# Performance work log

Hardware: AMD Instinct MI355X
Metric: run time of the kernel (lower is better)

The kernel has to match this reference:

```python
import jax, jax.numpy as jnp
import numpy as np

M, T, D, H = 2, 2048, 1024, 16
HD = D // H
SCALE = 1.0 / np.sqrt(D).astype(np.float32)  # original divides by sqrt(emb_dim)


def setup_inputs() -> dict:
    key = jax.random.key(0)
    ks = jax.random.split(key, 8)
    def lin(k):
        kw, kb = jax.random.split(k)
        W = jax.random.normal(kw, (D, D), dtype=jnp.float32) * (1.0 / np.sqrt(D))
        b = jax.random.normal(kb, (D,), dtype=jnp.float32) * 0.01
        return W, b
    Wq, bq = lin(ks[0]); Wk, bk = lin(ks[1]); Wv, bv = lin(ks[2]); Wo, bo = lin(ks[3])
    Q = jax.random.normal(ks[4], (M, T, D), dtype=jnp.float32)
    K = jax.random.normal(ks[5], (M, T, D), dtype=jnp.float32)
    V = jax.random.normal(ks[6], (M, T, D), dtype=jnp.float32)
    mask = jnp.ones((M, 1, 1, T), dtype=jnp.int32)
    return {"Q": Q, "K": K, "V": V, "mask": mask,
            "Wq": Wq, "bq": bq, "Wk": Wk, "bk": bk,
            "Wv": Wv, "bv": bv, "Wo": Wo, "bo": bo}


def reference(Q, K, V, mask, Wq, bq, Wk, bk, Wv, bv, Wo, bo):
    m = Q.shape[0]
    # torch nn.Linear: y = x @ W.T + b
    q = (Q @ Wq.T + bq).reshape(m, -1, H, HD)  # (m, Tq, h, hd)
    k = (K @ Wk.T + bk).reshape(m, -1, H, HD)
    v = (V @ Wv.T + bv).reshape(m, -1, H, HD)
    energy = jnp.einsum('mqhd,mkhd->mhqk', q, k) * SCALE
    if mask is not None:
        energy = jnp.where(mask == 0, jnp.float32(-1e20), energy)
    attn = jax.nn.softmax(energy, axis=3)  # dropout is identity at inference
    out = jnp.einsum('mhqk,mkhd->mqhd', attn, v)  # (m, Tq, h, hd)
    concat = out.reshape(m, -1, H * HD)
    return concat @ Wo.T + bo
```

## Files before the change

kernel.cpp:

```cpp
#include <hip/hip_runtime.h>
#include <cstdint>
#include <cstddef>

#define T_SEQ 2048
#define D_EMB 1024
#define H_HEADS 16
#define MROWS 4096
#define SC2 (0.03125f * 1.44269504f)
#define MASKNEG (-1e30f)

typedef __attribute__((ext_vector_type(8))) short bf16x8;
typedef __attribute__((ext_vector_type(4))) float f32x4;
typedef __attribute__((ext_vector_type(16))) float f32x16;
typedef __attribute__((ext_vector_type(4))) unsigned short us4;

__device__ __forceinline__ unsigned short f2bf(float f) {
  union { float f; uint32_t u; } v; v.f = f;
  uint32_t u = v.u;
  return (unsigned short)((u + 0x7FFFu + ((u >> 16) & 1u)) >> 16);
}

__device__ __forceinline__ uint32_t cvtpk(float lo, float hi) {
  uint32_t r;
  asm("v_cvt_pk_bf16_f32 %0, %1, %2" : "=v"(r) : "v"(lo), "v"(hi));
  return r;
}

__device__ __forceinline__ float fexp2(float x) {
  float r;
  asm("v_exp_f32 %0, %1" : "=v"(r) : "v"(x));
  return r;
}

__device__ __forceinline__ void gl16(const void* g, void* l) {
  __builtin_amdgcn_global_load_lds(
      (const __attribute__((address_space(1))) unsigned int*)g,
      (__attribute__((address_space(3))) unsigned int*)l, 16, 0, 0);
}

__global__ __launch_bounds__(256) void cvt_all(
    const float* __restrict__ Q, const float* __restrict__ K, const float* __restrict__ V,
    const float* __restrict__ Wq, const float* __restrict__ Wk,
    const float* __restrict__ Wv, const float* __restrict__ Wo,
    unsigned short* __restrict__ Qb, unsigned short* __restrict__ Kb,
    unsigned short* __restrict__ Vb,
    unsigned short* __restrict__ Wqb, unsigned short* __restrict__ Wkb,
    unsigned short* __restrict__ Wvb, unsigned short* __restrict__ Wob) {
  int i = blockIdx.x * 256 + threadIdx.x;
  const float* src;
  unsigned short* dst;
  int j;
  if (i < 3145728) {
    int s = i >> 20;
    j = i & 1048575;
    src = (s == 0) ? Q : (s == 1) ? K : V;
    dst = (s == 0) ? Qb : (s == 1) ? Kb : Vb;
  } else {
    int k = i - 3145728;
    int s = k >> 18;
    j = k & 262143;
    src = (s == 0) ? Wq : (s == 1) ? Wk : (s == 2) ? Wv : Wo;
    dst = (s == 0) ? Wqb : (s == 1) ? Wkb : (s == 2) ? Wvb : Wob;
  }
  float4 f = ((const float4*)src)[j];
  us4 o;
  o[0] = f2bf(f.x); o[1] = f2bf(f.y); o[2] = f2bf(f.z); o[3] = f2bf(f.w);
  ((us4*)dst)[j] = o;
}

__global__ __launch_bounds__(256) void qkv_gemm(
    const unsigned short* __restrict__ Qb, const unsigned short* __restrict__ Kb,
    const unsigned short* __restrict__ Vb,
    const unsigned short* __restrict__ Wqb, const unsigned short* __restrict__ Wkb,
    const unsigned short* __restrict__ Wvb,
    const float* __restrict__ bq, const float* __restrict__ bk, const float* __restrict__ bv,
    unsigned short* __restrict__ qo, unsigned short* __restrict__ ko,
    unsigned short* __restrict__ vto) {
  const int swz = (blockIdx.x & 7) * 96 + (blockIdx.x >> 3);
  const int bx = swz & 7, by = (swz >> 3) & 31, z = swz >> 8;
  const unsigned short* A = (z == 0) ? Qb : (z == 1) ? Kb : Vb;
  const unsigned short* W = (z == 0) ? Wqb : (z == 1) ? Wkb : Wvb;
  const float* bias = (z == 0) ? bq : (z == 1) ? bk : bv;

  __shared__ __align__(16) unsigned short Asm[2][128 * 32];
  __shared__ __align__(16) unsigned short Bsm[2][128 * 32];

  const int tid = threadIdx.x;
  const int lane = tid & 63, w = tid >> 6;
  const int fq = lane >> 4, fr = lane & 15;
  const int brow = by * 128, bcol = bx * 128;
  const int wr = (w >> 1) * 64, wc = (w & 1) * 64;

  f32x4 acc[4][4] = {};

#define QKV_STAGE(buf, k0)                                                     \
  {                                                                            \
    _Pragma("unroll") for (int it = 0; it < 2; ++it) {                         \
      int idx = it * 256 + tid;                                                \
      int row = idx >> 2, ce = (idx & 3) * 8;                                  \
      gl16(&A[(size_t)(brow + row) * D_EMB + (k0) + ce],                       \
           (char*)Asm[buf] + idx * 16);                                        \
      gl16(&W[(size_t)(bcol + row) * D_EMB + (k0) + ce],                       \
           (char*)Bsm[buf] + idx * 16);                                        \
    }                                                                          \
  }

#define QKV_COMPUTE(buf)                                                       \
  {                                                                            \
    bf16x8 af[4], bfr[4];                                                      \
    _Pragma("unroll") for (int i = 0; i < 4; ++i)                              \
        af[i] = *(const bf16x8*)((const char*)Asm[buf] +                       \
                                 (wr + i * 16 + fr) * 64 + fq * 16);           \
    _Pragma("unroll") for (int j = 0; j < 4; ++j)                              \
        bfr[j] = *(const bf16x8*)((const char*)Bsm[buf] +                      \
                                  (wc + j * 16 + fr) * 64 + fq * 16);          \
    _Pragma("unroll") for (int i = 0; i < 4; ++i)                              \
        _Pragma("unroll") for (int j = 0; j < 4; ++j)                          \
            acc[i][j] = __builtin_amdgcn_mfma_f32_16x16x32_bf16(               \
                af[i], bfr[j], acc[i][j], 0, 0, 0);                            \
  }

  QKV_STAGE(0, 0);
  __syncthreads();
#pragma unroll 1
  for (int t = 0; t < 32; t += 2) {
    QKV_STAGE(1, (t + 1) * 32);
    QKV_COMPUTE(0);
    __syncthreads();
    if (t + 2 < 32) QKV_STAGE(0, (t + 2) * 32);
    QKV_COMPUTE(1);
    __syncthreads();
  }

#pragma unroll
  for (int i = 0; i < 4; ++i) {
#pragma unroll
    for (int j = 0; j < 4; ++j) {
      int r0 = brow + wr + i * 16 + fq * 4;
      int cc = bcol + wc + j * 16 + fr;
      float bb = bias[cc];
      if (z < 2) {
        unsigned short* O = (z == 0) ? qo : ko;
        float sc = (z == 0) ? SC2 : 1.0f;
#pragma unroll
        for (int q = 0; q < 4; ++q)
          O[(size_t)(r0 + q) * D_EMB + cc] = f2bf((acc[i][j][q] + bb) * sc);
      } else {
        int hh = cc >> 6, dd = cc & 63;
        int mm = r0 >> 11, tt = r0 & 2047;
        us4 pk;
#pragma unroll
        for (int q = 0; q < 4; ++q) pk[q] = f2bf(acc[i][j][q] + bb);
        *(us4*)&vto[((size_t)((mm * H_HEADS + hh) * 64 + dd)) * T_SEQ + tt] = pk;
      }
    }
  }
}

__global__ __launch_bounds__(256) void out_gemm(const unsigned short* __restrict__ Ab,
                                                const unsigned short* __restrict__ Wb,
                                                const float* __restrict__ bias,
                                                float* __restrict__ Out) {
  const int swz = (blockIdx.x & 7) * 64 + (blockIdx.x >> 3);
  const int bx = swz & 15, by = swz >> 4;

  __shared__ __align__(16) unsigned short Asm[2][128 * 32];
  __shared__ __align__(16) unsigned short Bsm[2][64 * 32];
  const int tid = threadIdx.x;
  const int lane = tid & 63, w = tid >> 6;
  const int fq = lane >> 4, fr = lane & 15;
  const int brow = by * 128, bcol = bx * 64;
  const int wr = w * 32;

  f32x4 acc[2][4] = {};

#define OUT_STAGE(buf, k0)                                                     \
  {                                                                            \
    _Pragma("unroll") for (int it = 0; it < 2; ++it) {                         \
      int idx = it * 256 + tid;                                                \
      int row = idx >> 2, ce = (idx & 3) * 8;                                  \
      gl16(&Ab[(size_t)(brow + row) * D_EMB + (k0) + ce],                      \
           (char*)Asm[buf] + idx * 16);                                        \
    }                                                                          \
    {                                                                          \
      int row = tid >> 2, ce = (tid & 3) * 8;                                  \
      gl16(&Wb[(size_t)(bcol + row) * D_EMB + (k0) + ce],                      \
           (char*)Bsm[buf] + tid * 16);                                        \
    }                                                                          \
  }

#define OUT_COMPUTE(buf)                                                       \
  {                                                                            \
    bf16x8 af[2], bfr[4];                                                      \
    _Pragma("unroll") for (int i = 0; i < 2; ++i)                              \
        af[i] = *(const bf16x8*)((const char*)Asm[buf] +                       \
                                 (wr + i * 16 + fr) * 64 + fq * 16);           \
    _Pragma("unroll") for (int j = 0; j < 4; ++j)                              \
        bfr[j] = *(const bf16x8*)((const char*)Bsm[buf] +                      \
                                  (j * 16 + fr) * 64 + fq * 16);               \
    _Pragma("unroll") for (int i = 0; i < 2; ++i)                              \
        _Pragma("unroll") for (int j = 0; j < 4; ++j)                          \
            acc[i][j] = __builtin_amdgcn_mfma_f32_16x16x32_bf16(               \
                af[i], bfr[j], acc[i][j], 0, 0, 0);                            \
  }

  OUT_STAGE(0, 0);
  __syncthreads();
#pragma unroll 1
  for (int t = 0; t < 32; t += 2) {
    OUT_STAGE(1, (t + 1) * 32);
    OUT_COMPUTE(0);
    __syncthreads();
    if (t + 2 < 32) OUT_STAGE(0, (t + 2) * 32);
    OUT_COMPUTE(1);
    __syncthreads();
  }

#pragma unroll
  for (int i = 0; i < 2; ++i)
#pragma unroll
    for (int j = 0; j < 4; ++j) {
      int r0 = brow + wr + i * 16 + fq * 4;
      int cc = bcol + j * 16 + fr;
      float bb = bias[cc];
#pragma unroll
      for (int q = 0; q < 4; ++q)
        Out[(size_t)(r0 + q) * D_EMB + cc] = acc[i][j][q] + bb;
    }
}

__global__ __launch_bounds__(256) void attn_fwd(const unsigned short* __restrict__ qb,
                                                const unsigned short* __restrict__ kb,
                                                const unsigned short* __restrict__ vtb,
                                                const int* __restrict__ maskg,
                                                unsigned short* __restrict__ outb) {
  const int swzb = (blockIdx.x & 7) * 64 + (blockIdx.x >> 3);
  const int qt = swzb & 15, h = (swzb >> 4) & 15, mI = swzb >> 8;
  const int tid = threadIdx.x;
  const int lane = tid & 63, w = tid >> 6;
  const int lq = lane & 31, h2 = lane >> 5;
  const int xk = (lq & 7) << 4;
  const int vx = (lq & 7) << 4;

  __shared__ __align__(16) unsigned short Ksm[128 * 64];
  __shared__ __align__(16) unsigned short Vsm[64 * 128];
  __shared__ __align__(16) char Pw[4][2304];
  __shared__ __align__(16) float Msm[128];
  __shared__ int moks[16];

  char* KsmB = (char*)Ksm;
  char* VsmB = (char*)Vsm;
  char* PwB = Pw[w];

  if (tid < 16) moks[tid] = 1;
  __syncthreads();
  {
    int bad = 0;
    const int4* mg = (const int4*)&maskg[mI * T_SEQ + tid * 8];
    int4 a = mg[0], b = mg[1];
    bad |= (a.x == 0) | (a.y == 0) | (a.z == 0) | (a.w == 0);
    bad |= (b.x == 0) | (b.y == 0) | (b.z == 0) | (b.w == 0);
    if (bad) moks[tid >> 4] = 0;
  }
  __syncthreads();
  int okbits = 0;
#pragma unroll
  for (int i = 0; i < 16; ++i) okbits |= (moks[i] != 0) << i;

  const int qrow = qt * 128 + w * 32 + lq;
  bf16x8 qf[4];
#pragma unroll
  for (int db = 0; db < 4; ++db)
    qf[db] = *(const bf16x8*)&qb[((size_t)(mI * T_SEQ) + qrow) * D_EMB + h * 64 + db * 16 + h2 * 8];

  f32x16 oacc[2] = {};
  f32x16 liv = {};

  const unsigned short* kpan = kb + (size_t)(mI * T_SEQ) * D_EMB + h * 64;
  const unsigned short* vpan = vtb + (size_t)(mI * H_HEADS + h) * 64 * T_SEQ;

#pragma unroll 1
  for (int k0 = 0; k0 < T_SEQ; k0 += 128) {
    const int ok = (okbits >> (k0 >> 7)) & 1;
#pragma unroll
    for (int it = 0; it < 4; ++it) {
      int idx = it * 256 + tid;
      int row = idx >> 3;
      int sb = ((idx & 7) * 16) ^ ((row & 7) << 4);
      gl16(kpan + (size_t)(k0 + row) * D_EMB + (sb >> 1), KsmB + idx * 16);
    }
#pragma unroll
    for (int it = 0; it < 4; ++it) {
      int idx = it * 256 + tid;
      int row = idx >> 4;
      int sb = ((idx & 15) * 16) ^ ((row & 7) << 4);
      gl16(vpan + (size_t)row * T_SEQ + k0 + (sb >> 1), VsmB + idx * 16);
    }
    if (!ok && tid < 128) Msm[tid] = (maskg[mI * T_SEQ + k0 + tid] == 0) ? MASKNEG : 0.f;
    __syncthreads();

#pragma unroll 1
    for (int kbk = 0; kbk < 4; ++kbk) {
      f32x16 sv = {};
      const char* kr = KsmB + (kbk * 32 + lq) * 128;
#pragma unroll
      for (int db = 0; db < 4; ++db) {
        bf16x8 kf = *(const bf16x8*)(kr + ((db * 32 + h2 * 16) ^ xk));
        sv = __builtin_amdgcn_mfma_f32_32x32x16_bf16(kf, qf[db], sv, 0, 0, 0);
      }
      if (!ok) {
#pragma unroll
        for (int rg = 0; rg < 4; ++rg) {
          f32x4 mk = *(const f32x4*)&Msm[kbk * 32 + rg * 8 + h2 * 4];
          sv[rg * 4 + 0] += mk[0]; sv[rg * 4 + 1] += mk[1];
          sv[rg * 4 + 2] += mk[2]; sv[rg * 4 + 3] += mk[3];
        }
      }
#pragma unroll
      for (int r = 0; r < 16; ++r) sv[r] = fexp2(sv[r]);
      liv += sv;
#pragma unroll
      for (int rg = 0; rg < 4; ++rg) {
        uint2 pw;
        pw.x = cvtpk(sv[rg * 4 + 0], sv[rg * 4 + 1]);
        pw.y = cvtpk(sv[rg * 4 + 2], sv[rg * 4 + 3]);
        *(uint2*)(PwB + lq * 72 + rg * 16 + h2 * 8) = pw;
      }
      bf16x8 pf[2];
#pragma unroll
      for (int s = 0; s < 2; ++s) {
        union { bf16x8 v; uint2 d[2]; } u;
        u.d[0] = *(const uint2*)(PwB + lq * 72 + s * 32 + h2 * 16);
        u.d[1] = *(const uint2*)(PwB + lq * 72 + s * 32 + h2 * 16 + 8);
        pf[s] = u.v;
      }
#pragma unroll
      for (int vb = 0; vb < 2; ++vb) {
        const char* vbase = VsmB + (vb * 32 + lq) * 256;
#pragma unroll
        for (int s = 0; s < 2; ++s) {
          bf16x8 vf = *(const bf16x8*)(vbase + ((kbk * 64 + s * 32 + h2 * 16) ^ vx));
          oacc[vb] = __builtin_amdgcn_mfma_f32_32x32x16_bf16(vf, pf[s], oacc[vb], 0, 0, 0);
        }
      }
    }
    __syncthreads();
  }

  float li = 0.f;
#pragma unroll
  for (int r = 0; r < 16; ++r) li += liv[r];
  li += __shfl_xor(li, 32);
  float inv = 1.f / li;
  size_t orow = (size_t)(mI * T_SEQ + qrow) * D_EMB + h * 64;
#pragma unroll
  for (int vb = 0; vb < 2; ++vb)
#pragma unroll
    for (int rg = 0; rg < 4; ++rg) {
      uint2 ow;
      ow.x = cvtpk(oacc[vb][rg * 4 + 0] * inv, oacc[vb][rg * 4 + 1] * inv);
      ow.y = cvtpk(oacc[vb][rg * 4 + 2] * inv, oacc[vb][rg * 4 + 3] * inv);
      *(uint2*)&outb[orow + vb * 32 + rg * 8 + h2 * 4] = ow;
    }
}

extern "C" void kernel_launch(void* const* d_in, const int* in_sizes, int n_in,
                              void* d_out, int out_size, void* d_ws, size_t ws_size,
                              hipStream_t stream) {
  const float* Q  = (const float*)d_in[0];
  const float* K  = (const float*)d_in[1];
  const float* V  = (const float*)d_in[2];
  const int* mask = (const int*)d_in[3];
  const float* Wq = (const float*)d_in[4];
  const float* bq = (const float*)d_in[5];
  const float* Wk = (const float*)d_in[6];
  const float* bk = (const float*)d_in[7];
  const float* Wv = (const float*)d_in[8];
  const float* bv = (const float*)d_in[9];
  const float* Wo = (const float*)d_in[10];
  const float* bo = (const float*)d_in[11];

  uint8_t* ws = (uint8_t*)d_ws;
  const size_t MB = 1u << 20;
  unsigned short* Wq_b = (unsigned short*)(ws + 0 * MB);
  unsigned short* Wk_b = (unsigned short*)(ws + 2 * MB);
  unsigned short* Wv_b = (unsigned short*)(ws + 4 * MB);
  unsigned short* Wo_b = (unsigned short*)(ws + 6 * MB);
  unsigned short* q_b  = (unsigned short*)(ws + 8 * MB);
  unsigned short* k_b  = (unsigned short*)(ws + 16 * MB);
  unsigned short* vt_b = (unsigned short*)(ws + 24 * MB);
  unsigned short* Qb   = (unsigned short*)(ws + 32 * MB);
  unsigned short* Kb   = (unsigned short*)(ws + 40 * MB);
  unsigned short* Vb   = (unsigned short*)(ws + 48 * MB);
  unsigned short* cc_b = (unsigned short*)(ws + 32 * MB);

  cvt_all<<<dim3(16384), dim3(256), 0, stream>>>(Q, K, V, Wq, Wk, Wv, Wo,
                                                 Qb, Kb, Vb, Wq_b, Wk_b, Wv_b, Wo_b);

  qkv_gemm<<<dim3(768), dim3(256), 0, stream>>>(
      Qb, Kb, Vb, Wq_b, Wk_b, Wv_b, bq, bk, bv, q_b, k_b, vt_b);

  attn_fwd<<<dim3(512), dim3(256), 0, stream>>>(
      q_b, k_b, vt_b, mask, cc_b);

  out_gemm<<<dim3(512), dim3(256), 0, stream>>>(
      cc_b, Wo_b, bo, (float*)d_out);
}
```

Measured before the change: 141.7 us.

## Fuse activation bf16 conversion into QKV GEMM and double-buffer attention K/V tiles

Drops the separate fp32-to-bf16 pass over Q/K/V. The QKV GEMM now loads fp32 activations straight into swizzled LDS and packs them to bf16 when building fragments, which removes a full read-write round trip of the activations. The attention kernel double-buffers its K/V/mask tiles so the next tile's loads overlap the current tile's compute. It also replaces the per-wave LDS round trip for the probability matrix with cross-half register shuffles. The cost is twice the LDS for the A tile in the GEMM and double the K/V LDS in attention, which may lower occupancy.

```diff
diff --git a/kernel.cpp b/kernel.cpp
--- a/kernel.cpp
+++ b/kernel.cpp
@@ -38,30 +38,15 @@
       (__attribute__((address_space(3))) unsigned int*)l, 16, 0, 0);
 }
 
-__global__ __launch_bounds__(256) void cvt_all(
-    const float* __restrict__ Q, const float* __restrict__ K, const float* __restrict__ V,
+__global__ __launch_bounds__(256) void cvt_w(
     const float* __restrict__ Wq, const float* __restrict__ Wk,
     const float* __restrict__ Wv, const float* __restrict__ Wo,
-    unsigned short* __restrict__ Qb, unsigned short* __restrict__ Kb,
-    unsigned short* __restrict__ Vb,
     unsigned short* __restrict__ Wqb, unsigned short* __restrict__ Wkb,
     unsigned short* __restrict__ Wvb, unsigned short* __restrict__ Wob) {
   int i = blockIdx.x * 256 + threadIdx.x;
-  const float* src;
-  unsigned short* dst;
-  int j;
-  if (i < 3145728) {
-    int s = i >> 20;
-    j = i & 1048575;
-    src = (s == 0) ? Q : (s == 1) ? K : V;
-    dst = (s == 0) ? Qb : (s == 1) ? Kb : Vb;
-  } else {
-    int k = i - 3145728;
-    int s = k >> 18;
-    j = k & 262143;
-    src = (s == 0) ? Wq : (s == 1) ? Wk : (s == 2) ? Wv : Wo;
-    dst = (s == 0) ? Wqb : (s == 1) ? Wkb : (s == 2) ? Wvb : Wob;
-  }
+  int s = i >> 18, j = i & 262143;
+  const float* src = (s == 0) ? Wq : (s == 1) ? Wk : (s == 2) ? Wv : Wo;
+  unsigned short* dst = (s == 0) ? Wqb : (s == 1) ? Wkb : (s == 2) ? Wvb : Wob;
   float4 f = ((const float4*)src)[j];
   us4 o;
   o[0] = f2bf(f.x); o[1] = f2bf(f.y); o[2] = f2bf(f.z); o[3] = f2bf(f.w);
@@ -69,8 +54,8 @@
 }
 
 __global__ __launch_bounds__(256) void qkv_gemm(
-    const unsigned short* __restrict__ Qb, const unsigned short* __restrict__ Kb,
-    const unsigned short* __restrict__ Vb,
+    const float* __restrict__ Qf, const float* __restrict__ Kf,
+    const float* __restrict__ Vf,
     const unsigned short* __restrict__ Wqb, const unsigned short* __restrict__ Wkb,
     const unsigned short* __restrict__ Wvb,
     const float* __restrict__ bq, const float* __restrict__ bk, const float* __restrict__ bv,
@@ -78,11 +63,11 @@
     unsigned short* __restrict__ vto) {
   const int swz = (blockIdx.x & 7) * 96 + (blockIdx.x >> 3);
   const int bx = swz & 7, by = (swz >> 3) & 31, z = swz >> 8;
-  const unsigned short* A = (z == 0) ? Qb : (z == 1) ? Kb : Vb;
+  const float* A = (z == 0) ? Qf : (z == 1) ? Kf : Vf;
   const unsigned short* W = (z == 0) ? Wqb : (z == 1) ? Wkb : Wvb;
   const float* bias = (z == 0) ? bq : (z == 1) ? bk : bv;
 
-  __shared__ __align__(16) unsigned short Asm[2][128 * 32];
+  __shared__ __align__(16) float Asm[2][128 * 32];
   __shared__ __align__(16) unsigned short Bsm[2][128 * 32];
 
   const int tid = threadIdx.x;
@@ -95,11 +80,16 @@
 
 #define QKV_STAGE(buf, k0)                                                     \
   {                                                                            \
+    _Pragma("unroll") for (int it = 0; it < 4; ++it) {                         \
+      int idx = it * 256 + tid;                                                \
+      int row = idx >> 3;                                                      \
+      int sb = ((idx & 7) * 16) ^ ((row & 7) << 4);                            \
+      gl16(&A[(size_t)(brow + row) * D_EMB + (k0) + (sb >> 2)],                \
+           (char*)Asm[buf] + idx * 16);                                        \
+    }                                                                          \
     _Pragma("unroll") for (int it = 0; it < 2; ++it) {                         \
       int idx = it * 256 + tid;                                                \
       int row = idx >> 2, ce = (idx & 3) * 8;                                  \
-      gl16(&A[(size_t)(brow + row) * D_EMB + (k0) + ce],                       \
-           (char*)Asm[buf] + idx * 16);                                        \
       gl16(&W[(size_t)(bcol + row) * D_EMB + (k0) + ce],                       \
            (char*)Bsm[buf] + idx * 16);                                        \
     }                                                                          \
@@ -108,9 +98,17 @@
 #define QKV_COMPUTE(buf)                                                       \
   {                                                                            \
     bf16x8 af[4], bfr[4];                                                      \
-    _Pragma("unroll") for (int i = 0; i < 4; ++i)                              \
-        af[i] = *(const bf16x8*)((const char*)Asm[buf] +                       \
-                                 (wr + i * 16 + fr) * 64 + fq * 16);           \
+    _Pragma("unroll") for (int i = 0; i < 4; ++i) {                            \
+      int row = wr + i * 16 + fr;                                              \
+      int x = (row & 7) << 4;                                                  \
+      const char* base = (const char*)Asm[buf] + row * 128;                    \
+      f32x4 lo = *(const f32x4*)(base + ((fq * 32) ^ x));                      \
+      f32x4 hi = *(const f32x4*)(base + ((fq * 32 + 16) ^ x));                 \
+      union { bf16x8 v; uint32_t u[4]; } a_;                                   \
+      a_.u[0] = cvtpk(lo[0], lo[1]); a_.u[1] = cvtpk(lo[2], lo[3]);            \
+      a_.u[2] = cvtpk(hi[0], hi[1]); a_.u[3] = cvtpk(hi[2], hi[3]);            \
+      af[i] = a_.v;                                                            \
+    }                                                                          \
     _Pragma("unroll") for (int j = 0; j < 4; ++j)                              \
         bfr[j] = *(const bf16x8*)((const char*)Bsm[buf] +                      \
                                   (wc + j * 16 + fr) * 64 + fq * 16);          \
@@ -242,15 +240,10 @@
   const int xk = (lq & 7) << 4;
   const int vx = (lq & 7) << 4;
 
-  __shared__ __align__(16) unsigned short Ksm[128 * 64];
-  __shared__ __align__(16) unsigned short Vsm[64 * 128];
-  __shared__ __align__(16) char Pw[4][2304];
-  __shared__ __align__(16) float Msm[128];
+  __shared__ __align__(16) unsigned short Ksm[2][128 * 64];
+  __shared__ __align__(16) unsigned short Vsm[2][64 * 128];
+  __shared__ __align__(16) float Msm[2][128];
   __shared__ int moks[16];
-
-  char* KsmB = (char*)Ksm;
-  char* VsmB = (char*)Vsm;
-  char* PwB = Pw[w];
 
   if (tid < 16) moks[tid] = 1;
   __syncthreads();
@@ -279,70 +272,90 @@
   const unsigned short* kpan = kb + (size_t)(mI * T_SEQ) * D_EMB + h * 64;
   const unsigned short* vpan = vtb + (size_t)(mI * H_HEADS + h) * 64 * T_SEQ;
 
+#define ATTN_STAGE(buf, t)                                                     \
+  {                                                                            \
+    int k0s = (t) * 128;                                                       \
+    _Pragma("unroll") for (int it = 0; it < 4; ++it) {                         \
+      int idx = it * 256 + tid;                                                \
+      int row = idx >> 3;                                                      \
+      int sb = ((idx & 7) * 16) ^ ((row & 7) << 4);                            \
+      gl16(kpan + (size_t)(k0s + row) * D_EMB + (sb >> 1),                     \
+           (char*)Ksm[buf] + idx * 16);                                        \
+    }                                                                          \
+    _Pragma("unroll") for (int it = 0; it < 4; ++it) {                         \
+      int idx = it * 256 + tid;                                                \
+      int row = idx >> 4;                                                      \
+      int sb = ((idx & 15) * 16) ^ ((row & 7) << 4);                           \
+      gl16(vpan + (size_t)row * T_SEQ + k0s + (sb >> 1),                       \
+           (char*)Vsm[buf] + idx * 16);                                        \
+    }                                                                          \
+    if (!((okbits >> (t)) & 1) && tid < 128)                                   \
+      Msm[buf][tid] = (maskg[mI * T_SEQ + k0s + tid] == 0) ? MASKNEG : 0.f;    \
+  }
+
+#define ATTN_COMPUTE(buf, okv)                                                 \
+  _Pragma("unroll 1") for (int kbk = 0; kbk < 4; ++kbk) {                      \
+    f32x16 sv = {};                                                            \
+    const char* kr = (const char*)Ksm[buf] + (kbk * 32 + lq) * 128;            \
+    _Pragma("unroll") for (int db = 0; db < 4; ++db) {                         \
+      bf16x8 kf = *(const bf16x8*)(kr + ((db * 32 + h2 * 16) ^ xk));           \
+      sv = __builtin_amdgcn_mfma_f32_32x32x16_bf16(kf, qf[db], sv, 0, 0, 0);   \
+    }                                                                          \
+    if (!(okv)) {                                                              \
+      _Pragma("unroll") for (int rg = 0; rg < 4; ++rg) {                       \
+        f32x4 mk = *(const f32x4*)&Msm[buf][kbk * 32 + rg * 8 + h2 * 4];       \
+        sv[rg * 4 + 0] += mk[0]; sv[rg * 4 + 1] += mk[1];                      \
+        sv[rg * 4 + 2] += mk[2]; sv[rg * 4 + 3] += mk[3];                      \
+      }                                                                        \
+    }                                                                          \
+    _Pragma("unroll") for (int r = 0; r < 16; ++r) sv[r] = fexp2(sv[r]);       \
+    liv += sv;                                                                 \
+    uint32_t w0 = cvtpk(sv[0], sv[1]), w1 = cvtpk(sv[2], sv[3]);               \
+    uint32_t w2 = cvtpk(sv[4], sv[5]), w3 = cvtpk(sv[6], sv[7]);               \
+    uint32_t w4 = cvtpk(sv[8], sv[9]), w5 = cvtpk(sv[10], sv[11]);             \
+    uint32_t w6 = cvtpk(sv[12], sv[13]), w7 = cvtpk(sv[14], sv[15]);           \
+    uint32_t x0 = __shfl_xor(w0, 32), x1 = __shfl_xor(w1, 32);                 \
+    uint32_t x2 = __shfl_xor(w2, 32), x3 = __shfl_xor(w3, 32);                 \
+    uint32_t x4 = __shfl_xor(w4, 32), x5 = __shfl_xor(w5, 32);                 \
+    uint32_t x6 = __shfl_xor(w6, 32), x7 = __shfl_xor(w7, 32);                 \
+    bf16x8 pf[2];                                                              \
+    {                                                                          \
+      union { bf16x8 v; uint32_t u[4]; } u_;                                   \
+      u_.u[0] = h2 ? x2 : w0; u_.u[1] = h2 ? x3 : w1;                          \
+      u_.u[2] = h2 ? w2 : x0; u_.u[3] = h2 ? w3 : x1;                          \
+      pf[0] = u_.v;                                                            \
+    }                                                                          \
+    {                                                                          \
+      union { bf16x8 v; uint32_t u[4]; } u_;                                   \
+      u_.u[0] = h2 ? x6 : w4; u_.u[1] = h2 ? x7 : w5;                          \
+      u_.u[2] = h2 ? w6 : x4; u_.u[3] = h2 ? w7 : x5;                          \
+      pf[1] = u_.v;                                                            \
+    }                                                                          \
+    _Pragma("unroll") for (int vb = 0; vb < 2; ++vb) {                         \
+      const char* vbase = (const char*)Vsm[buf] + (vb * 32 + lq) * 256;        \
+      _Pragma("unroll") for (int s = 0; s < 2; ++s) {                          \
+        bf16x8 vf = *(const bf16x8*)(vbase +                                   \
+                        ((kbk * 64 + s * 32 + h2 * 16) ^ vx));                 \
+        oacc[vb] = __builtin_amdgcn_mfma_f32_32x32x16_bf16(                    \
+            vf, pf[s], oacc[vb], 0, 0, 0);                                     \
+      }                                                                        \
+    }                                                                          \
+  }
+
+  ATTN_STAGE(0, 0);
+  __syncthreads();
 #pragma unroll 1
-  for (int k0 = 0; k0 < T_SEQ; k0 += 128) {
-    const int ok = (okbits >> (k0 >> 7)) & 1;
-#pragma unroll
-    for (int it = 0; it < 4; ++it) {
-      int idx = it * 256 + tid;
-      int row = idx >> 3;
-      int sb = ((idx & 7) * 16) ^ ((row & 7) << 4);
-      gl16(kpan + (size_t)(k0 + row) * D_EMB + (sb >> 1), KsmB + idx * 16);
+  for (int t = 0; t < 16; t += 2) {
+    ATTN_STAGE(1, t + 1);
+    {
+      const int okv = (okbits >> t) & 1;
+      ATTN_COMPUTE(0, okv);
     }
-#pragma unroll
-    for (int it = 0; it < 4; ++it) {
-      int idx = it * 256 + tid;
-      int row = idx >> 4;
-      int sb = ((idx & 15) * 16) ^ ((row & 7) << 4);
-      gl16(vpan + (size_t)row * T_SEQ + k0 + (sb >> 1), VsmB + idx * 16);
-    }
-    if (!ok && tid < 128) Msm[tid] = (maskg[mI * T_SEQ + k0 + tid] == 0) ? MASKNEG : 0.f;
-    __syncthreads();
-
-#pragma unroll 1
-    for (int kbk = 0; kbk < 4; ++kbk) {
-      f32x16 sv = {};
-      const char* kr = KsmB + (kbk * 32 + lq) * 128;
-#pragma unroll
-      for (int db = 0; db < 4; ++db) {
-        bf16x8 kf = *(const bf16x8*)(kr + ((db * 32 + h2 * 16) ^ xk));
-        sv = __builtin_amdgcn_mfma_f32_32x32x16_bf16(kf, qf[db], sv, 0, 0, 0);
-      }
-      if (!ok) {
-#pragma unroll
-        for (int rg = 0; rg < 4; ++rg) {
-          f32x4 mk = *(const f32x4*)&Msm[kbk * 32 + rg * 8 + h2 * 4];
-          sv[rg * 4 + 0] += mk[0]; sv[rg * 4 + 1] += mk[1];
-          sv[rg * 4 + 2] += mk[2]; sv[rg * 4 + 3] += mk[3];
-        }
-      }
-#pragma unroll
-      for (int r = 0; r < 16; ++r) sv[r] = fexp2(sv[r]);
-      liv += sv;
-#pragma unroll
-      for (int rg = 0; rg < 4; ++rg) {
-        uint2 pw;
-        pw.x = cvtpk(sv[rg * 4 + 0], sv[rg * 4 + 1]);
-        pw.y = cvtpk(sv[rg * 4 + 2], sv[rg * 4 + 3]);
-        *(uint2*)(PwB + lq * 72 + rg * 16 + h2 * 8) = pw;
-      }
-      bf16x8 pf[2];
-#pragma unroll
-      for (int s = 0; s < 2; ++s) {
-        union { bf16x8 v; uint2 d[2]; } u;
-        u.d[0] = *(const uint2*)(PwB + lq * 72 + s * 32 + h2 * 16);
-        u.d[1] = *(const uint2*)(PwB + lq * 72 + s * 32 + h2 * 16 + 8);
-        pf[s] = u.v;
-      }
-#pragma unroll
-      for (int vb = 0; vb < 2; ++vb) {
-        const char* vbase = VsmB + (vb * 32 + lq) * 256;
-#pragma unroll
-        for (int s = 0; s < 2; ++s) {
-          bf16x8 vf = *(const bf16x8*)(vbase + ((kbk * 64 + s * 32 + h2 * 16) ^ vx));
-          oacc[vb] = __builtin_amdgcn_mfma_f32_32x32x16_bf16(vf, pf[s], oacc[vb], 0, 0, 0);
-        }
-      }
+    __syncthreads();
+    if (t + 2 < 16) ATTN_STAGE(0, t + 2);
+    {
+      const int okv = (okbits >> (t + 1)) & 1;
+      ATTN_COMPUTE(1, okv);
     }
     __syncthreads();
   }
@@ -389,16 +402,13 @@
   unsigned short* q_b  = (unsigned short*)(ws + 8 * MB);
   unsigned short* k_b  = (unsigned short*)(ws + 16 * MB);
   unsigned short* vt_b = (unsigned short*)(ws + 24 * MB);
-  unsigned short* Qb   = (unsigned short*)(ws + 32 * MB);
-  unsigned short* Kb   = (unsigned short*)(ws + 40 * MB);
-  unsigned short* Vb   = (unsigned short*)(ws + 48 * MB);
   unsigned short* cc_b = (unsigned short*)(ws + 32 * MB);
 
-  cvt_all<<<dim3(16384), dim3(256), 0, stream>>>(Q, K, V, Wq, Wk, Wv, Wo,
-                                                 Qb, Kb, Vb, Wq_b, Wk_b, Wv_b, Wo_b);
+  cvt_w<<<dim3(4096), dim3(256), 0, stream>>>(Wq, Wk, Wv, Wo,
+                                              Wq_b, Wk_b, Wv_b, Wo_b);
 
   qkv_gemm<<<dim3(768), dim3(256), 0, stream>>>(
-      Qb, Kb, Vb, Wq_b, Wk_b, Wv_b, bq, bk, bv, q_b, k_b, vt_b);
+      Q, K, V, Wq_b, Wk_b, Wv_b, bq, bk, bv, q_b, k_b, vt_b);
 
   attn_fwd<<<dim3(512), dim3(256), 0, stream>>>(
       q_b, k_b, vt_b, mask, cc_b);
```

After: 142.4 us. No clear change (+0.5%).
